# Kernel optimization log

Measured on AMD Instinct MI355X. Metric: run time of the kernel, lower is better.

## Reference

```python
import jax, jax.numpy as jnp
import numpy as np

B, S, D, H = 4, 2048, 512, 8
DK = D // H
SCALE = 1.0 / np.sqrt(DK)


def setup_inputs() -> dict:
    key = jax.random.key(0)
    kx, kq, kk, kv = jax.random.split(key, 4)
    w_std = np.sqrt(2.0 / (D + D))  # xavier-ish scale
    return {
        "x": jax.random.normal(kx, (B, S, D), dtype=jnp.float32),
        "W_Q": jax.random.normal(kq, (D, D), dtype=jnp.float32) * w_std,
        "W_K": jax.random.normal(kk, (D, D), dtype=jnp.float32) * w_std,
        "W_V": jax.random.normal(kv, (D, D), dtype=jnp.float32) * w_std,
    }


def reference(x, W_Q, W_K, W_V):
    # torch Linear(bias=False): y = x @ W.T
    q = jnp.einsum('bsd,ed->bse', x, W_Q).reshape(B, S, H, DK).transpose(0, 2, 1, 3)
    k = jnp.einsum('bsd,ed->bse', x, W_K).reshape(B, S, H, DK).transpose(0, 2, 1, 3)
    v = jnp.einsum('bsd,ed->bse', x, W_V).reshape(B, S, H, DK).transpose(0, 2, 1, 3)
    scores = jnp.einsum('bhqd,bhkd->bhqk', q, k) * SCALE  # [B,H,S,S]
    scores_exp = jnp.exp(scores)  # faithful: no max-subtraction in original
    attn = scores_exp / (scores_exp.sum(axis=-1, keepdims=True) + 1e-8)
    context = jnp.einsum('bhqk,bhkd->bhqd', attn, v)
    return context.transpose(0, 2, 1, 3).reshape(B, S, D)
```

## Files before the change

kernel.cpp:

```cpp
#include <hip/hip_runtime.h>
#include <hip/hip_bf16.h>

#define Bsz 4
#define Ssz 2048
#define Dsz 512
#define Hsz 8
#define DKsz 64

typedef __bf16 bf16x8 __attribute__((ext_vector_type(8)));
typedef __bf16 bf16x4 __attribute__((ext_vector_type(4)));
typedef float f32x4 __attribute__((ext_vector_type(4)));

#define SWE(c, row) ((((c) ^ ((row) & 7)) * 8))

__global__ __launch_bounds__(256) void cvt_kernel(
    const float* __restrict__ x, const float* __restrict__ Wq,
    const float* __restrict__ Wk, const float* __restrict__ Wv,
    __bf16* __restrict__ xb, __bf16* __restrict__ Wb)
{
    const int i = blockIdx.x * 256 + threadIdx.x;
    const int XN4 = (Bsz * Ssz * Dsz) / 4;
    const float* src;
    __bf16* dst;
    int off;
    if (i < XN4) {
        src = x; dst = xb; off = i;
    } else {
        int j = i - XN4;
        int w = j >> 16;
        off = j & 65535;
        src = (w == 0) ? Wq : (w == 1) ? Wk : Wv;
        dst = Wb + (size_t)w * (Dsz * Dsz);
    }
    float4 v = ((const float4*)src)[off];
    __bf16 o[4] = {(__bf16)v.x, (__bf16)v.y, (__bf16)v.z, (__bf16)v.w};
    *(uint2*)(dst + (size_t)off * 4) = *(uint2*)o;
}

__global__ __launch_bounds__(256, 3) void qkv_kernel(
    const __bf16* __restrict__ xb, const __bf16* __restrict__ Wb,
    __bf16* __restrict__ Qo, __bf16* __restrict__ Ko, __bf16* __restrict__ Vo)
{
    __shared__ __bf16 xs[128][64];
    __shared__ __bf16 wsh[128][64];

    const int tid  = threadIdx.x;
    const int lane = tid & 63;
    const int wave = tid >> 6;
    const int quad = lane >> 4;
    const int l16  = lane & 15;
    const int wm   = (wave & 1) * 64;
    const int wn   = (wave >> 1) * 64;

    const int lin = blockIdx.x;
    const int xcd = lin & 7;
    const int idx = lin >> 3;
    const int tnw = idx % 12;
    const int tmh = idx / 12;
    const int tm  = (tmh * 8 + xcd) * 128;
    const int tn  = (tnw & 3) * 128;
    const int which = tnw >> 2;
    const bool VM = (which == 2);
    const __bf16* W = Wb + (size_t)which * (Dsz * Dsz);

    const int srow = tid >> 3;
    const int sc   = tid & 7;
    const int swz  = SWE(sc, srow);

    const __bf16* xg = xb + (size_t)(tm + srow) * Dsz + sc * 8;
    const __bf16* wg = W  + (size_t)(tn + srow) * Dsz + sc * 8;

    bf16x8 px[4], pw[4];
    #pragma unroll
    for (int i = 0; i < 4; ++i) {
        px[i] = *(const bf16x8*)(xg + (size_t)(32 * i) * Dsz);
        pw[i] = *(const bf16x8*)(wg + (size_t)(32 * i) * Dsz);
    }

    f32x4 acc[4][4];
    #pragma unroll
    for (int i = 0; i < 4; ++i)
        #pragma unroll
        for (int j = 0; j < 4; ++j) acc[i][j] = (f32x4){0.f, 0.f, 0.f, 0.f};

    const __bf16 (*Ash)[64] = VM ? xs : wsh;
    const __bf16 (*Bsh)[64] = VM ? wsh : xs;

    for (int k0 = 0; k0 < Dsz; k0 += 64) {
        __syncthreads();
        #pragma unroll
        for (int i = 0; i < 4; ++i) {
            *(bf16x8*)&xs[srow + 32 * i][swz]  = px[i];
            *(bf16x8*)&wsh[srow + 32 * i][swz] = pw[i];
        }
        __syncthreads();
        if (k0 + 64 < Dsz) {
            #pragma unroll
            for (int i = 0; i < 4; ++i) {
                px[i] = *(const bf16x8*)(xg + (size_t)(32 * i) * Dsz + k0 + 64);
                pw[i] = *(const bf16x8*)(wg + (size_t)(32 * i) * Dsz + k0 + 64);
            }
        }

        #pragma unroll
        for (int kk = 0; kk < 2; ++kk) {
            bf16x8 fa[4], fb[4];
            #pragma unroll
            for (int mi = 0; mi < 4; ++mi) {
                const int row = wm + mi * 16 + l16;
                fa[mi] = *(const bf16x8*)&Ash[row][SWE(kk * 4 + quad, row)];
            }
            #pragma unroll
            for (int ni = 0; ni < 4; ++ni) {
                const int row = wn + ni * 16 + l16;
                fb[ni] = *(const bf16x8*)&Bsh[row][SWE(kk * 4 + quad, row)];
            }
            #pragma unroll
            for (int mi = 0; mi < 4; ++mi)
                #pragma unroll
                for (int ni = 0; ni < 4; ++ni)
                    acc[mi][ni] = __builtin_amdgcn_mfma_f32_16x16x32_bf16(
                        fa[mi], fb[ni], acc[mi][ni], 0, 0, 0);
        }
    }

    if (!VM) {
        const float scale = (which == 0) ? 0.125f * 1.44269504088896340736f : 1.0f;
        __bf16* dst = (which == 0) ? Qo : Ko;
        #pragma unroll
        for (int mi = 0; mi < 4; ++mi) {
            const int e0 = tn + wm + mi * 16 + quad * 4;
            const int h = e0 >> 6, d0 = e0 & 63;
            #pragma unroll
            for (int ni = 0; ni < 4; ++ni) {
                const int sf = tm + wn + ni * 16 + l16;
                const int b = sf >> 11, s = sf & (Ssz - 1);
                bf16x4 p;
                #pragma unroll
                for (int r = 0; r < 4; ++r) p[r] = (__bf16)(acc[mi][ni][r] * scale);
                *(bf16x4*)&dst[((((size_t)(b * Hsz + h) * Ssz + s)) << 6) + d0] = p;
            }
        }
    } else {
        #pragma unroll
        for (int mi = 0; mi < 4; ++mi) {
            const int sf0 = tm + wm + mi * 16 + quad * 4;
            const int b = sf0 >> 11, s0 = sf0 & (Ssz - 1);
            #pragma unroll
            for (int ni = 0; ni < 4; ++ni) {
                const int e = tn + wn + ni * 16 + l16;
                const int h = e >> 6, d = e & 63;
                bf16x4 p;
                #pragma unroll
                for (int r = 0; r < 4; ++r) p[r] = (__bf16)acc[mi][ni][r];
                *(bf16x4*)&Vo[(((size_t)(b * Hsz + h) * DKsz + d) << 11) + s0] = p;
            }
        }
    }
}

__global__ __launch_bounds__(256, 2) void attn_kernel(
    const __bf16* __restrict__ Q, const __bf16* __restrict__ K,
    const __bf16* __restrict__ VT, float* __restrict__ out)
{
    __shared__ __bf16 ks[64][64];
    __shared__ __bf16 vs[64][64];
    __shared__ __bf16 ps[4][16][64];

    const int tid  = threadIdx.x;
    const int lane = tid & 63;
    const int wave = tid >> 6;
    const int quad = lane >> 4;
    const int l16  = lane & 15;

    const int bh = blockIdx.x;
    const int qt = blockIdx.y;
    const int b  = bh >> 3;
    const int h  = bh & 7;

    const __bf16* Qb = Q  + (size_t)bh * Ssz * DKsz;
    const __bf16* Kb = K  + (size_t)bh * Ssz * DKsz;
    const __bf16* Vb = VT + (size_t)bh * DKsz * Ssz;

    bf16x8 qf[2][2];
    #pragma unroll
    for (int qs = 0; qs < 2; ++qs) {
        const __bf16* qrow = Qb + (size_t)(qt * 128 + wave * 32 + qs * 16 + l16) * DKsz;
        qf[qs][0] = *(const bf16x8*)(qrow + quad * 8);
        qf[qs][1] = *(const bf16x8*)(qrow + 32 + quad * 8);
    }

    bf16x8 ones;
    #pragma unroll
    for (int i = 0; i < 8; ++i) ones[i] = (__bf16)1.0f;

    f32x4 oacc[2][4];
    #pragma unroll
    for (int qs = 0; qs < 2; ++qs)
        #pragma unroll
        for (int i = 0; i < 4; ++i) oacc[qs][i] = (f32x4){0.f, 0.f, 0.f, 0.f};
    f32x4 lacc[2] = {(f32x4){0.f, 0.f, 0.f, 0.f}, (f32x4){0.f, 0.f, 0.f, 0.f}};

    const int srow = tid >> 3;
    const int sc   = tid & 7;
    const int swz  = SWE(sc, srow);

    const __bf16* kg = Kb + (size_t)srow * DKsz + sc * 8;
    const __bf16* vg = Vb + (size_t)srow * Ssz + sc * 8;

    bf16x8 pk0 = *(const bf16x8*)(kg);
    bf16x8 pk1 = *(const bf16x8*)(kg + (size_t)32 * DKsz);
    bf16x8 pv0 = *(const bf16x8*)(vg);
    bf16x8 pv1 = *(const bf16x8*)(vg + (size_t)32 * Ssz);

    for (int kb = 0; kb < Ssz; kb += 64) {
        __syncthreads();
        *(bf16x8*)&ks[srow][swz]      = pk0;
        *(bf16x8*)&ks[srow + 32][swz] = pk1;
        *(bf16x8*)&vs[srow][swz]      = pv0;
        *(bf16x8*)&vs[srow + 32][swz] = pv1;
        __syncthreads();

        if (kb + 64 < Ssz) {
            pk0 = *(const bf16x8*)(kg + (size_t)(kb + 64) * DKsz);
            pk1 = *(const bf16x8*)(kg + (size_t)(kb + 96) * DKsz);
            pv0 = *(const bf16x8*)(vg + kb + 64);
            pv1 = *(const bf16x8*)(vg + (size_t)32 * Ssz + kb + 64);
        }

        bf16x8 kf[2][4], vf[2][4];
        #pragma unroll
        for (int kk = 0; kk < 2; ++kk)
            #pragma unroll
            for (int ns = 0; ns < 4; ++ns) {
                const int row = ns * 16 + l16;
                kf[kk][ns] = *(const bf16x8*)&ks[row][SWE(kk * 4 + quad, row)];
                vf[kk][ns] = *(const bf16x8*)&vs[row][SWE(kk * 4 + quad, row)];
            }

        #pragma unroll
        for (int qs = 0; qs < 2; ++qs) {
            #pragma unroll
            for (int ns = 0; ns < 4; ++ns) {
                f32x4 st = (f32x4){0.f, 0.f, 0.f, 0.f};
                st = __builtin_amdgcn_mfma_f32_16x16x32_bf16(kf[0][ns], qf[qs][0], st, 0, 0, 0);
                st = __builtin_amdgcn_mfma_f32_16x16x32_bf16(kf[1][ns], qf[qs][1], st, 0, 0, 0);
                bf16x4 pp;
                #pragma unroll
                for (int r = 0; r < 4; ++r)
                    pp[r] = (__bf16)__builtin_amdgcn_exp2f(st[r]);
                const int c = ns * 2 + (quad >> 1);
                *(bf16x4*)&ps[wave][l16][((c ^ (l16 & 7)) << 3) + ((quad & 1) << 2)] = pp;
            }
            bf16x8 af0 = *(const bf16x8*)&ps[wave][l16][SWE(quad, l16)];
            bf16x8 af1 = *(const bf16x8*)&ps[wave][l16][SWE(4 + quad, l16)];
            #pragma unroll
            for (int ns = 0; ns < 4; ++ns) {
                oacc[qs][ns] = __builtin_amdgcn_mfma_f32_16x16x32_bf16(vf[0][ns], af0, oacc[qs][ns], 0, 0, 0);
                oacc[qs][ns] = __builtin_amdgcn_mfma_f32_16x16x32_bf16(vf[1][ns], af1, oacc[qs][ns], 0, 0, 0);
            }
            lacc[qs] = __builtin_amdgcn_mfma_f32_16x16x32_bf16(ones, af0, lacc[qs], 0, 0, 0);
            lacc[qs] = __builtin_amdgcn_mfma_f32_16x16x32_bf16(ones, af1, lacc[qs], 0, 0, 0);
        }
    }

    #pragma unroll
    for (int qs = 0; qs < 2; ++qs) {
        const float linv = 1.f / (lacc[qs][0] + 1e-8f);
        const int q = qt * 128 + wave * 32 + qs * 16 + l16;
        float* obase = out + ((size_t)b * Ssz + q) * Dsz + h * DKsz;
        #pragma unroll
        for (int ns = 0; ns < 4; ++ns) {
            f32x4 o = oacc[qs][ns] * linv;
            *(f32x4*)(obase + ns * 16 + quad * 4) = o;
        }
    }
}

extern "C" void kernel_launch(void* const* d_in, const int* in_sizes, int n_in,
                              void* d_out, int out_size, void* d_ws, size_t ws_size,
                              hipStream_t stream) {
    const float* x  = (const float*)d_in[0];
    const float* Wq = (const float*)d_in[1];
    const float* Wk = (const float*)d_in[2];
    const float* Wv = (const float*)d_in[3];
    float* out = (float*)d_out;

    const size_t per = (size_t)Bsz * Hsz * Ssz * DKsz;
    __bf16* Qw  = (__bf16*)d_ws;
    __bf16* Kw  = Qw + per;
    __bf16* VTw = Kw + per;
    __bf16* xb  = VTw + per;
    __bf16* Wb  = xb + per;

    cvt_kernel<<<4864, 256, 0, stream>>>(x, Wq, Wk, Wv, xb, Wb);
    qkv_kernel<<<768, 256, 0, stream>>>(xb, Wb, Qw, Kw, VTw);
    attn_kernel<<<dim3(Bsz * Hsz, Ssz / 128), 256, 0, stream>>>(Qw, Kw, VTw, out);
}
```

Baseline: 137.9 us.

## Shrink attention query tile to 64 rows, raise occupancy, add MFMA priority hints

The attention kernel now gives each wave 16 query rows instead of 32, so a block covers 64 queries and the grid doubles. Launch bounds rise from 2 to 4 blocks per CU. K/V fragments are read from shared memory just before use instead of being preloaded into registers. The MFMA phases are wrapped in s_setprio to favour matrix issue. Together these cut register pressure so more waves can hide latency, at the cost of loading each K/V tile twice as often per query.

```diff
diff --git a/kernel.cpp b/kernel.cpp
--- a/kernel.cpp
+++ b/kernel.cpp
@@ -159,7 +159,7 @@
     }
 }
 
-__global__ __launch_bounds__(256, 2) void attn_kernel(
+__global__ __launch_bounds__(256, 4) void attn_kernel(
     const __bf16* __restrict__ Q, const __bf16* __restrict__ K,
     const __bf16* __restrict__ VT, float* __restrict__ out)
 {
@@ -182,24 +182,21 @@
     const __bf16* Kb = K  + (size_t)bh * Ssz * DKsz;
     const __bf16* Vb = VT + (size_t)bh * DKsz * Ssz;
 
-    bf16x8 qf[2][2];
-    #pragma unroll
-    for (int qs = 0; qs < 2; ++qs) {
-        const __bf16* qrow = Qb + (size_t)(qt * 128 + wave * 32 + qs * 16 + l16) * DKsz;
-        qf[qs][0] = *(const bf16x8*)(qrow + quad * 8);
-        qf[qs][1] = *(const bf16x8*)(qrow + 32 + quad * 8);
+    bf16x8 qf[2];
+    {
+        const __bf16* qrow = Qb + (size_t)(qt * 64 + wave * 16 + l16) * DKsz;
+        qf[0] = *(const bf16x8*)(qrow + quad * 8);
+        qf[1] = *(const bf16x8*)(qrow + 32 + quad * 8);
     }
 
     bf16x8 ones;
     #pragma unroll
     for (int i = 0; i < 8; ++i) ones[i] = (__bf16)1.0f;
 
-    f32x4 oacc[2][4];
-    #pragma unroll
-    for (int qs = 0; qs < 2; ++qs)
-        #pragma unroll
-        for (int i = 0; i < 4; ++i) oacc[qs][i] = (f32x4){0.f, 0.f, 0.f, 0.f};
-    f32x4 lacc[2] = {(f32x4){0.f, 0.f, 0.f, 0.f}, (f32x4){0.f, 0.f, 0.f, 0.f}};
+    f32x4 oacc[4];
+    #pragma unroll
+    for (int i = 0; i < 4; ++i) oacc[i] = (f32x4){0.f, 0.f, 0.f, 0.f};
+    f32x4 lacc = (f32x4){0.f, 0.f, 0.f, 0.f};
 
     const int srow = tid >> 3;
     const int sc   = tid & 7;
@@ -228,50 +225,53 @@
             pv1 = *(const bf16x8*)(vg + (size_t)32 * Ssz + kb + 64);
         }
 
-        bf16x8 kf[2][4], vf[2][4];
-        #pragma unroll
-        for (int kk = 0; kk < 2; ++kk)
-            #pragma unroll
-            for (int ns = 0; ns < 4; ++ns) {
-                const int row = ns * 16 + l16;
-                kf[kk][ns] = *(const bf16x8*)&ks[row][SWE(kk * 4 + quad, row)];
-                vf[kk][ns] = *(const bf16x8*)&vs[row][SWE(kk * 4 + quad, row)];
-            }
-
-        #pragma unroll
-        for (int qs = 0; qs < 2; ++qs) {
-            #pragma unroll
-            for (int ns = 0; ns < 4; ++ns) {
-                f32x4 st = (f32x4){0.f, 0.f, 0.f, 0.f};
-                st = __builtin_amdgcn_mfma_f32_16x16x32_bf16(kf[0][ns], qf[qs][0], st, 0, 0, 0);
-                st = __builtin_amdgcn_mfma_f32_16x16x32_bf16(kf[1][ns], qf[qs][1], st, 0, 0, 0);
-                bf16x4 pp;
-                #pragma unroll
-                for (int r = 0; r < 4; ++r)
-                    pp[r] = (__bf16)__builtin_amdgcn_exp2f(st[r]);
-                const int c = ns * 2 + (quad >> 1);
-                *(bf16x4*)&ps[wave][l16][((c ^ (l16 & 7)) << 3) + ((quad & 1) << 2)] = pp;
-            }
-            bf16x8 af0 = *(const bf16x8*)&ps[wave][l16][SWE(quad, l16)];
-            bf16x8 af1 = *(const bf16x8*)&ps[wave][l16][SWE(4 + quad, l16)];
-            #pragma unroll
-            for (int ns = 0; ns < 4; ++ns) {
-                oacc[qs][ns] = __builtin_amdgcn_mfma_f32_16x16x32_bf16(vf[0][ns], af0, oacc[qs][ns], 0, 0, 0);
-                oacc[qs][ns] = __builtin_amdgcn_mfma_f32_16x16x32_bf16(vf[1][ns], af1, oacc[qs][ns], 0, 0, 0);
-            }
-            lacc[qs] = __builtin_amdgcn_mfma_f32_16x16x32_bf16(ones, af0, lacc[qs], 0, 0, 0);
-            lacc[qs] = __builtin_amdgcn_mfma_f32_16x16x32_bf16(ones, af1, lacc[qs], 0, 0, 0);
-        }
-    }
-
-    #pragma unroll
-    for (int qs = 0; qs < 2; ++qs) {
-        const float linv = 1.f / (lacc[qs][0] + 1e-8f);
-        const int q = qt * 128 + wave * 32 + qs * 16 + l16;
+        f32x4 st[4];
+        __builtin_amdgcn_s_setprio(1);
+        #pragma unroll
+        for (int ns = 0; ns < 4; ++ns) {
+            const int row = ns * 16 + l16;
+            const bf16x8 k0 = *(const bf16x8*)&ks[row][SWE(quad, row)];
+            const bf16x8 k1 = *(const bf16x8*)&ks[row][SWE(4 + quad, row)];
+            f32x4 t = (f32x4){0.f, 0.f, 0.f, 0.f};
+            t = __builtin_amdgcn_mfma_f32_16x16x32_bf16(k0, qf[0], t, 0, 0, 0);
+            t = __builtin_amdgcn_mfma_f32_16x16x32_bf16(k1, qf[1], t, 0, 0, 0);
+            st[ns] = t;
+        }
+        __builtin_amdgcn_s_setprio(0);
+
+        #pragma unroll
+        for (int ns = 0; ns < 4; ++ns) {
+            bf16x4 pp;
+            #pragma unroll
+            for (int r = 0; r < 4; ++r)
+                pp[r] = (__bf16)__builtin_amdgcn_exp2f(st[ns][r]);
+            const int c = ns * 2 + (quad >> 1);
+            *(bf16x4*)&ps[wave][l16][((c ^ (l16 & 7)) << 3) + ((quad & 1) << 2)] = pp;
+        }
+        const bf16x8 af0 = *(const bf16x8*)&ps[wave][l16][SWE(quad, l16)];
+        const bf16x8 af1 = *(const bf16x8*)&ps[wave][l16][SWE(4 + quad, l16)];
+
+        __builtin_amdgcn_s_setprio(1);
+        #pragma unroll
+        for (int ns = 0; ns < 4; ++ns) {
+            const int row = ns * 16 + l16;
+            const bf16x8 v0 = *(const bf16x8*)&vs[row][SWE(quad, row)];
+            const bf16x8 v1 = *(const bf16x8*)&vs[row][SWE(4 + quad, row)];
+            oacc[ns] = __builtin_amdgcn_mfma_f32_16x16x32_bf16(v0, af0, oacc[ns], 0, 0, 0);
+            oacc[ns] = __builtin_amdgcn_mfma_f32_16x16x32_bf16(v1, af1, oacc[ns], 0, 0, 0);
+        }
+        lacc = __builtin_amdgcn_mfma_f32_16x16x32_bf16(ones, af0, lacc, 0, 0, 0);
+        lacc = __builtin_amdgcn_mfma_f32_16x16x32_bf16(ones, af1, lacc, 0, 0, 0);
+        __builtin_amdgcn_s_setprio(0);
+    }
+
+    {
+        const float linv = 1.f / (lacc[0] + 1e-8f);
+        const int q = qt * 64 + wave * 16 + l16;
         float* obase = out + ((size_t)b * Ssz + q) * Dsz + h * DKsz;
         #pragma unroll
         for (int ns = 0; ns < 4; ++ns) {
-            f32x4 o = oacc[qs][ns] * linv;
+            f32x4 o = oacc[ns] * linv;
             *(f32x4*)(obase + ns * 16 + quad * 4) = o;
         }
     }
@@ -295,5 +295,5 @@
 
     cvt_kernel<<<4864, 256, 0, stream>>>(x, Wq, Wk, Wv, xb, Wb);
     qkv_kernel<<<768, 256, 0, stream>>>(xb, Wb, Qw, Kw, VTw);
-    attn_kernel<<<dim3(Bsz * Hsz, Ssz / 128), 256, 0, stream>>>(Qw, Kw, VTw, out);
-}
+    attn_kernel<<<dim3(Bsz * Hsz, Ssz / 64), 256, 0, stream>>>(Qw, Kw, VTw, out);
+}
```

Result: slower. 147.2 us (+6.7%).

## Load projection tiles straight into LDS and prioritize MFMA phases in attention

Applied to the files above, without the earlier changes.

The QKV projection GEMM now uses global_load_lds to copy x and W tiles directly from global memory into LDS, with a lane-level XOR swizzle on the source address. This replaces the register-staged prefetch of the next k-tile. It waits on vmcnt(0) before the barrier, so the previous overlap of loads for the next tile with the current MFMAs is lost. In the attention kernel, the QK^T MFMAs are grouped before the exp2 stage, and s_setprio raises wave priority around the MFMA blocks to improve interleaving between waves.

```diff
diff --git a/kernel.cpp b/kernel.cpp
--- a/kernel.cpp
+++ b/kernel.cpp
@@ -12,6 +12,10 @@
 typedef float f32x4 __attribute__((ext_vector_type(4)));
 
 #define SWE(c, row) ((((c) ^ ((row) & 7)) * 8))
+
+#define GLL16(g, l) __builtin_amdgcn_global_load_lds(                      \
+    (const __attribute__((address_space(1))) void*)(g),                    \
+    (__attribute__((address_space(3))) void*)(l), 16, 0, 0)
 
 __global__ __launch_bounds__(256) void cvt_kernel(
     const float* __restrict__ x, const float* __restrict__ Wq,
@@ -63,19 +67,10 @@
     const bool VM = (which == 2);
     const __bf16* W = Wb + (size_t)which * (Dsz * Dsz);
 
-    const int srow = tid >> 3;
-    const int sc   = tid & 7;
-    const int swz  = SWE(sc, srow);
-
-    const __bf16* xg = xb + (size_t)(tm + srow) * Dsz + sc * 8;
-    const __bf16* wg = W  + (size_t)(tn + srow) * Dsz + sc * 8;
-
-    bf16x8 px[4], pw[4];
-    #pragma unroll
-    for (int i = 0; i < 4; ++i) {
-        px[i] = *(const bf16x8*)(xg + (size_t)(32 * i) * Dsz);
-        pw[i] = *(const bf16x8*)(wg + (size_t)(32 * i) * Dsz);
-    }
+    const int rl  = lane >> 3;
+    const int gch = (lane & 7) ^ rl;
+    const __bf16* xsrc = xb + (size_t)(tm + wave * 8 + rl) * Dsz + gch * 8;
+    const __bf16* wsrc = W  + (size_t)(tn + wave * 8 + rl) * Dsz + gch * 8;
 
     f32x4 acc[4][4];
     #pragma unroll
@@ -90,17 +85,11 @@
         __syncthreads();
         #pragma unroll
         for (int i = 0; i < 4; ++i) {
-            *(bf16x8*)&xs[srow + 32 * i][swz]  = px[i];
-            *(bf16x8*)&wsh[srow + 32 * i][swz] = pw[i];
-        }
-        __syncthreads();
-        if (k0 + 64 < Dsz) {
-            #pragma unroll
-            for (int i = 0; i < 4; ++i) {
-                px[i] = *(const bf16x8*)(xg + (size_t)(32 * i) * Dsz + k0 + 64);
-                pw[i] = *(const bf16x8*)(wg + (size_t)(32 * i) * Dsz + k0 + 64);
-            }
-        }
+            GLL16(xsrc + (size_t)(32 * i) * Dsz + k0, &xs[wave * 8 + 32 * i][0]);
+            GLL16(wsrc + (size_t)(32 * i) * Dsz + k0, &wsh[wave * 8 + 32 * i][0]);
+        }
+        asm volatile("s_waitcnt vmcnt(0)" ::: "memory");
+        __syncthreads();
 
         #pragma unroll
         for (int kk = 0; kk < 2; ++kk) {
@@ -240,20 +229,30 @@
 
         #pragma unroll
         for (int qs = 0; qs < 2; ++qs) {
-            #pragma unroll
-            for (int ns = 0; ns < 4; ++ns) {
-                f32x4 st = (f32x4){0.f, 0.f, 0.f, 0.f};
-                st = __builtin_amdgcn_mfma_f32_16x16x32_bf16(kf[0][ns], qf[qs][0], st, 0, 0, 0);
-                st = __builtin_amdgcn_mfma_f32_16x16x32_bf16(kf[1][ns], qf[qs][1], st, 0, 0, 0);
+            __builtin_amdgcn_s_setprio(1);
+            f32x4 st[4];
+            #pragma unroll
+            for (int ns = 0; ns < 4; ++ns) {
+                f32x4 t = (f32x4){0.f, 0.f, 0.f, 0.f};
+                t = __builtin_amdgcn_mfma_f32_16x16x32_bf16(kf[0][ns], qf[qs][0], t, 0, 0, 0);
+                t = __builtin_amdgcn_mfma_f32_16x16x32_bf16(kf[1][ns], qf[qs][1], t, 0, 0, 0);
+                st[ns] = t;
+            }
+            __builtin_amdgcn_s_setprio(0);
+
+            #pragma unroll
+            for (int ns = 0; ns < 4; ++ns) {
                 bf16x4 pp;
                 #pragma unroll
                 for (int r = 0; r < 4; ++r)
-                    pp[r] = (__bf16)__builtin_amdgcn_exp2f(st[r]);
+                    pp[r] = (__bf16)__builtin_amdgcn_exp2f(st[ns][r]);
                 const int c = ns * 2 + (quad >> 1);
                 *(bf16x4*)&ps[wave][l16][((c ^ (l16 & 7)) << 3) + ((quad & 1) << 2)] = pp;
             }
-            bf16x8 af0 = *(const bf16x8*)&ps[wave][l16][SWE(quad, l16)];
-            bf16x8 af1 = *(const bf16x8*)&ps[wave][l16][SWE(4 + quad, l16)];
+            const bf16x8 af0 = *(const bf16x8*)&ps[wave][l16][SWE(quad, l16)];
+            const bf16x8 af1 = *(const bf16x8*)&ps[wave][l16][SWE(4 + quad, l16)];
+
+            __builtin_amdgcn_s_setprio(1);
             #pragma unroll
             for (int ns = 0; ns < 4; ++ns) {
                 oacc[qs][ns] = __builtin_amdgcn_mfma_f32_16x16x32_bf16(vf[0][ns], af0, oacc[qs][ns], 0, 0, 0);
@@ -261,6 +260,7 @@
             }
             lacc[qs] = __builtin_amdgcn_mfma_f32_16x16x32_bf16(ones, af0, lacc[qs], 0, 0, 0);
             lacc[qs] = __builtin_amdgcn_mfma_f32_16x16x32_bf16(ones, af1, lacc[qs], 0, 0, 0);
+            __builtin_amdgcn_s_setprio(0);
         }
     }
 
```

After: 134.4 us. -2.5%, faster.
